# Performance work log

Measured on AMD Instinct MI355X. Metric: run time of the kernel, lower is better.

The kernel has to match this reference:

```python
import jax, jax.numpy as jnp
import numpy as np

EMB = 2048
NQH = 16          # num_q_heads
G = 4             # group_size
NKV = NQH // G    # 4 kv heads
HD = EMB // NQH   # 128 head_dim
B, S = 2, 2048


def setup_inputs() -> dict:
    key = jax.random.key(0)
    ks = jax.random.split(key, 6)
    scale = 1.0 / np.sqrt(EMB)
    x = jax.random.normal(ks[0], (B, S, EMB), dtype=jnp.float32)
    attn_mask = jnp.zeros((B, S), dtype=bool)  # unused placeholder
    # torch Linear weights: (out_features, in_features)
    Wq = jax.random.normal(ks[1], (EMB, EMB), dtype=jnp.float32) * scale
    Wk = jax.random.normal(ks[2], (EMB // G, EMB), dtype=jnp.float32) * scale
    Wv = jax.random.normal(ks[3], (EMB // G, EMB), dtype=jnp.float32) * scale
    Wo = jax.random.normal(ks[4], (EMB, EMB), dtype=jnp.float32) * scale
    return {"x": x, "attn_mask": attn_mask, "is_causal": 1,
            "Wq": Wq, "Wk": Wk, "Wv": Wv, "Wo": Wo}


def reference(x, attn_mask, is_causal, Wq, Wk, Wv, Wo):
    b, n, _ = x.shape
    q = x @ Wq.T                      # (b, n, EMB)
    k = x @ Wk.T                      # (b, n, EMB//G)
    v = x @ Wv.T                      # (b, n, EMB//G)
    # q: b n (h_full d) -> b h_full n d, then (h g) split with h=NKV outer
    q = q.reshape(b, n, NQH, HD).transpose(0, 2, 1, 3)      # (b, NQH, n, d)
    q = q.reshape(b, NKV, G, n, HD).transpose(0, 2, 1, 3, 4)  # (b, g, h, n, d)
    k = k.reshape(b, n, NKV, HD).transpose(0, 2, 1, 3)      # (b, h, s, d)
    v = v.reshape(b, n, NKV, HD).transpose(0, 2, 1, 3)      # (b, h, s, d)
    attn = jnp.einsum('bghnd,bhsd->bghns', q, k) / np.sqrt(HD)
    scores = jax.nn.softmax(attn, axis=-1)  # dropout p=0.0 -> identity
    out = jnp.einsum('bghns,bhsd->bghnd', scores, v)        # (b, g, h, n, d)
    # b g h n d -> b n (h g) d -> b n (h g d)
    out = out.transpose(0, 3, 2, 1, 4).reshape(b, n, EMB)
    y = out @ Wo.T
    return y
```

## Files before the change

### kernel.cpp

```cpp
#include <hip/hip_runtime.h>
#include <stdint.h>


typedef short s8v __attribute__((ext_vector_type(8)));
typedef float f4  __attribute__((ext_vector_type(4)));
typedef unsigned short u16;

#define GLD_LDS(g, l) __builtin_amdgcn_global_load_lds(                     \
    (const __attribute__((address_space(1))) void*)(g),                     \
    (__attribute__((address_space(3))) void*)(l), 16, 0, 0)

__device__ __forceinline__ u16 f2bf(float f) {
    union { float f; uint32_t u; } v; v.f = f;
    uint32_t u = v.u;
    return (u16)((u + 0x7fffu + ((u >> 16) & 1u)) >> 16);
}

__device__ __forceinline__ float fexp2(float x) {
#if __has_builtin(__builtin_amdgcn_exp2f)
    return __builtin_amdgcn_exp2f(x);
#else
    return exp2f(x);
#endif
}

__global__ void cvt_all(const float* __restrict__ x,  const float* __restrict__ wq,
                        const float* __restrict__ wk, const float* __restrict__ wv,
                        const float* __restrict__ wo_,
                        u16* __restrict__ xb, u16* __restrict__ wqkv,
                        u16* __restrict__ wob)
{
    int i = blockIdx.x * blockDim.x + threadIdx.x;
    const float4* s; ushort4* d; int so, dofs;
    if (i < 2097152)      { s = (const float4*)x;   d = (ushort4*)xb;   so = i;           dofs = so; }
    else if (i < 3145728) { s = (const float4*)wq;  d = (ushort4*)wqkv; so = i - 2097152; dofs = so; }
    else if (i < 3407872) { s = (const float4*)wk;  d = (ushort4*)wqkv; so = i - 3145728; dofs = so + 1048576; }
    else if (i < 3670016) { s = (const float4*)wv;  d = (ushort4*)wqkv; so = i - 3407872; dofs = so + 1310720; }
    else                  { s = (const float4*)wo_; d = (ushort4*)wob;  so = i - 3670016; dofs = so; }
    float4 v = s[so];
    ushort4 o;
    o.x = f2bf(v.x); o.y = f2bf(v.y); o.z = f2bf(v.z); o.w = f2bf(v.w);
    d[dofs] = o;
}

template<int MODE>
__global__ __launch_bounds__(512, 1)
void gemm256(const u16* __restrict__ A, const u16* __restrict__ Bm,
             int M, int N, int K,
             u16* __restrict__ qkOut, u16* __restrict__ vtOut,
             float* __restrict__ fOut)
{
    __shared__ __attribute__((aligned(16))) u16 lds[2][2][2][8192];

    const int tid  = threadIdx.x;
    const int lane = tid & 63, quad = lane >> 4, l16 = lane & 15;
    const int wave = tid >> 6;
    const int wr = wave >> 2, wc = wave & 3;

    int bx, by;
    {
        const int nwgx = gridDim.x;
        const int nwg  = nwgx * gridDim.y;
        const int flat = blockIdx.y * nwgx + blockIdx.x;
        const int nflat = (flat & 7) * (nwg >> 3) + (flat >> 3);
        bx = nflat % nwgx; by = nflat / nwgx;
    }
    const int m0 = by * 256, n0 = bx * 256;
    const int NT = K >> 6;

    f4 acc[8][4] = {};

#define VMC6() asm volatile("s_waitcnt vmcnt(6)" ::: "memory")
#define VMC0() asm volatile("s_waitcnt vmcnt(0)" ::: "memory")
#define BAR()  __builtin_amdgcn_s_barrier()

#define STG(bf, op, h, t) if ((t) < NT) {                                   \
        const u16* gb = (op) ? Bm : A;                                      \
        const int rb = ((op) ? n0 : m0) + (h) * 128;                        \
        _Pragma("unroll")                                                   \
        for (int j = 0; j < 2; j++) {                                       \
            int s_ = j * 512 + tid;                                         \
            int r_ = s_ >> 3, cc = s_ & 7;                                  \
            GLD_LDS(gb + (size_t)(rb + r_) * K + (t) * 64                   \
                       + ((cc ^ (r_ & 7)) << 3),                            \
                    &lds[bf][op][h][(j * 512 + (tid & ~63)) * 8]);          \
        } }

#define RD_A(bf, qm, ar) {                                                  \
        _Pragma("unroll")                                                   \
        for (int f = 0; f < 4; f++) {                                       \
            int r_ = (qm) * 64 + f * 16 + l16;                              \
            _Pragma("unroll")                                               \
            for (int kc = 0; kc < 2; kc++)                                  \
                ar[f][kc] = *(const s8v*)(&lds[bf][0][wr]                   \
                    [r_ * 64 + (((kc * 4 + quad) ^ (r_ & 7)) << 3)]);       \
        } }

#define RD_B(bf, qn, br) {                                                  \
        _Pragma("unroll")                                                   \
        for (int f = 0; f < 2; f++) {                                       \
            int r_ = (wc & 1) * 64 + ((qn) * 2 + f) * 16 + l16;             \
            _Pragma("unroll")                                               \
            for (int kc = 0; kc < 2; kc++)                                  \
                br[f][kc] = *(const s8v*)(&lds[bf][1][wc >> 1]              \
                    [r_ * 64 + (((kc * 4 + quad) ^ (r_ & 7)) << 3)]);       \
        } }

#define MM(qm, qn, ar, br) {                                                \
        __builtin_amdgcn_s_setprio(1);                                      \
        _Pragma("unroll")                                                   \
        for (int f = 0; f < 4; f++)                                         \
            _Pragma("unroll")                                               \
            for (int g = 0; g < 2; g++) {                                   \
                acc[(qm)*4+f][(qn)*2+g] = __builtin_amdgcn_mfma_f32_16x16x32_bf16( \
                    ar[f][0], br[g][0], acc[(qm)*4+f][(qn)*2+g], 0, 0, 0);  \
                acc[(qm)*4+f][(qn)*2+g] = __builtin_amdgcn_mfma_f32_16x16x32_bf16( \
                    ar[f][1], br[g][1], acc[(qm)*4+f][(qn)*2+g], 0, 0, 0);  \
            }                                                               \
        __builtin_amdgcn_s_setprio(0); }

    STG(0,1,0,0); STG(0,1,1,0); STG(0,0,0,0); STG(0,0,1,0);
    STG(1,1,0,1); STG(1,1,1,1); STG(1,0,0,1);
    VMC6(); BAR();

    for (int T = 0; T < NT; T += 2) {
        const bool more = (T + 2 < NT);
        s8v a0[4][2], a1[4][2], b0[2][2], b1[2][2];
        RD_A(0,0,a0); RD_B(0,0,b0);
        STG(1,0,1,T+1);
        BAR(); MM(0,0,a0,b0); BAR();
        RD_B(0,1,b1);
        BAR(); MM(0,1,a0,b1); BAR();
        RD_A(0,1,a1);
        STG(0,1,0,T+2);
        BAR(); MM(1,0,a1,b0); BAR();
        STG(0,1,1,T+2); STG(0,0,0,T+2);
        BAR(); MM(1,1,a1,b1);
        if (more) { VMC6(); } else { VMC0(); }
        BAR();
        RD_A(1,0,a0); RD_B(1,0,b0);
        STG(0,0,1,T+2);
        BAR(); MM(0,0,a0,b0); BAR();
        RD_B(1,1,b1);
        BAR(); MM(0,1,a0,b1); BAR();
        RD_A(1,1,a1);
        STG(1,1,0,T+3);
        BAR(); MM(1,0,a1,b0); BAR();
        STG(1,1,1,T+3); STG(1,0,0,T+3);
        BAR(); MM(1,1,a1,b1);
        if (more) { VMC6(); } else { VMC0(); }
        BAR();
    }
#undef STG
#undef RD_A
#undef RD_B
#undef MM

    if (MODE == 0) {
        if (n0 < 2560) {
            const float qs = (n0 < 2048)
                ? (0.08838834764831845f * 1.4426950408889634f) : 1.0f;
            #pragma unroll
            for (int mi = 0; mi < 8; mi++) {
                int gm0 = m0 + wr * 128 + mi * 16 + quad * 4;
                #pragma unroll
                for (int ni = 0; ni < 4; ni++) {
                    int gn = n0 + wc * 64 + ni * 16 + l16;
                    #pragma unroll
                    for (int r = 0; r < 4; r++)
                        qkOut[(size_t)(gm0 + r) * 2560 + gn] = f2bf(acc[mi][ni][r] * qs);
                }
            }
        } else {
            #pragma unroll
            for (int mi = 0; mi < 8; mi++) {
                int gm0 = m0 + wr * 128 + mi * 16 + quad * 4;
                int bb = gm0 >> 11, s = gm0 & 2047;
                #pragma unroll
                for (int ni = 0; ni < 4; ni++) {
                    int gn = n0 + wc * 64 + ni * 16 + l16;
                    int dd = gn - 2560;
                    ushort4 pk;
                    pk.x = f2bf(acc[mi][ni][0]); pk.y = f2bf(acc[mi][ni][1]);
                    pk.z = f2bf(acc[mi][ni][2]); pk.w = f2bf(acc[mi][ni][3]);
                    *(ushort4*)(vtOut +
                        ((size_t)(bb * 4 + (dd >> 7)) * 128 + (dd & 127)) * 2048 + s) = pk;
                }
            }
        }
    } else {
        #pragma unroll
        for (int mi = 0; mi < 8; mi++) {
            int gm0 = m0 + wr * 128 + mi * 16 + quad * 4;
            #pragma unroll
            for (int ni = 0; ni < 4; ni++) {
                int gn = n0 + wc * 64 + ni * 16 + l16;
                #pragma unroll
                for (int r = 0; r < 4; r++)
                    fOut[(size_t)(gm0 + r) * N + gn] = acc[mi][ni][r];
            }
        }
    }
#undef VMC6
#undef VMC0
#undef BAR
}

__global__ __launch_bounds__(512, 1)
void gemm256x128(const u16* __restrict__ A, const u16* __restrict__ Bm,
                 int M, int N, int K, float* __restrict__ fOut)
{
    __shared__ __attribute__((aligned(16))) u16 lds[2][3][8192];

    const int tid  = threadIdx.x;
    const int lane = tid & 63, quad = lane >> 4, l16 = lane & 15;
    const int wave = tid >> 6;
    const int wr = wave >> 2, wc = wave & 3;

    int bx, by;
    {
        const int nwgx = gridDim.x;
        const int nwg  = nwgx * gridDim.y;
        const int flat = blockIdx.y * nwgx + blockIdx.x;
        const int nflat = (flat & 7) * (nwg >> 3) + (flat >> 3);
        bx = nflat % nwgx; by = nflat / nwgx;
    }
    const int m0 = by * 256, n0 = bx * 128;
    const int NT = K >> 6;

    f4 acc[8][2] = {};

#define VMC2() asm volatile("s_waitcnt vmcnt(2)" ::: "memory")
#define VMC0() asm volatile("s_waitcnt vmcnt(0)" ::: "memory")
#define BAR()  __builtin_amdgcn_s_barrier()

#define STG(bf, u, t) if ((t) < NT) {                                       \
        const u16* gb = ((u) == 2) ? Bm : A;                                \
        const int rb = ((u) == 2) ? n0 : (m0 + (u) * 128);                  \
        _Pragma("unroll")                                                   \
        for (int j = 0; j < 2; j++) {                                       \
            int s_ = j * 512 + tid;                                         \
            int r_ = s_ >> 3, cc = s_ & 7;                                  \
            GLD_LDS(gb + (size_t)(rb + r_) * K + (t) * 64                   \
                       + ((cc ^ (r_ & 7)) << 3),                            \
                    &lds[bf][u][(j * 512 + (tid & ~63)) * 8]);              \
        } }

#define RD_A(bf, qm, ar) {                                                  \
        _Pragma("unroll")                                                   \
        for (int f = 0; f < 4; f++) {                                       \
            int r_ = (qm) * 64 + f * 16 + l16;                              \
            _Pragma("unroll")                                               \
            for (int kc = 0; kc < 2; kc++)                                  \
                ar[f][kc] = *(const s8v*)(&lds[bf][wr]                      \
                    [r_ * 64 + (((kc * 4 + quad) ^ (r_ & 7)) << 3)]);       \
        } }

#define RD_B(bf, br) {                                                      \
        _Pragma("unroll")                                                   \
        for (int f = 0; f < 2; f++) {                                       \
            int r_ = wc * 32 + f * 16 + l16;                                \
            _Pragma("unroll")                                               \
            for (int kc = 0; kc < 2; kc++)                                  \
                br[f][kc] = *(const s8v*)(&lds[bf][2]                       \
                    [r_ * 64 + (((kc * 4 + quad) ^ (r_ & 7)) << 3)]);       \
        } }

#define MM(qm, ar, br) {                                                    \
        __builtin_amdgcn_s_setprio(1);                                      \
        _Pragma("unroll")                                                   \
        for (int f = 0; f < 4; f++)                                         \
            _Pragma("unroll")                                               \
            for (int g = 0; g < 2; g++) {                                   \
                acc[(qm)*4+f][g] = __builtin_amdgcn_mfma_f32_16x16x32_bf16( \
                    ar[f][0], br[g][0], acc[(qm)*4+f][g], 0, 0, 0);         \
                acc[(qm)*4+f][g] = __builtin_amdgcn_mfma_f32_16x16x32_bf16( \
                    ar[f][1], br[g][1], acc[(qm)*4+f][g], 0, 0, 0);         \
            }                                                               \
        __builtin_amdgcn_s_setprio(0); }

    STG(0,0,0); STG(0,1,0); STG(0,2,0);
    STG(1,2,1);
    VMC2(); BAR();

    for (int T = 0; T < NT; T += 2) {
        const bool more = (T + 2 < NT);
        s8v a0[4][2], a1[4][2], b[2][2];
        RD_A(0,0,a0); RD_B(0,b);
        STG(1,0,T+1); STG(1,1,T+1);
        BAR(); MM(0,a0,b); BAR();
        RD_A(0,1,a1);
        STG(0,2,T+2);
        BAR(); MM(1,a1,b);
        if (more) { VMC2(); } else { VMC0(); }
        BAR();
        RD_A(1,0,a0); RD_B(1,b);
        STG(0,0,T+2); STG(0,1,T+2);
        BAR(); MM(0,a0,b); BAR();
        RD_A(1,1,a1);
        STG(1,2,T+3);
        BAR(); MM(1,a1,b);
        if (more) { VMC2(); } else { VMC0(); }
        BAR();
    }
#undef STG
#undef RD_A
#undef RD_B
#undef MM
#undef VMC2
#undef VMC0
#undef BAR

    #pragma unroll
    for (int mi = 0; mi < 8; mi++) {
        int gm0 = m0 + wr * 128 + mi * 16 + quad * 4;
        #pragma unroll
        for (int ni = 0; ni < 2; ni++) {
            int gn = n0 + wc * 32 + ni * 16 + l16;
            #pragma unroll
            for (int r = 0; r < 4; r++)
                fOut[(size_t)(gm0 + r) * N + gn] = acc[mi][ni][r];
        }
    }
}

__global__ __launch_bounds__(512, 2)
void attn_kernel(const u16* __restrict__ qk, const u16* __restrict__ vt,
                 u16* __restrict__ ao)
{
    __shared__ __attribute__((aligned(16))) u16 Kb[2][64 * 128];
    __shared__ __attribute__((aligned(16))) u16 Vb[2][128 * 64];
    __shared__ __attribute__((aligned(16))) u16 Ps[8][32 * 72];

    const int tid  = threadIdx.x;
    const int wave = tid >> 6, lane = tid & 63;
    const int quad = lane >> 4, l16 = lane & 15;
    const int bh = blockIdx.x;
    const int b = bh >> 2, h = bh & 3;
    const int hh = wave >> 1, mh = wave & 1;
    const int hq = h * 4 + hh;
    const int qs0 = blockIdx.y * 64;

    s8v aq[2][4];
    #pragma unroll
    for (int mt = 0; mt < 2; mt++) {
        const u16* qrow = qk + (size_t)(b * 2048 + qs0 + (mh * 2 + mt) * 16 + l16) * 2560
                             + hq * 128 + quad * 8;
        #pragma unroll
        for (int c4 = 0; c4 < 4; c4++) aq[mt][c4] = *(const s8v*)(qrow + c4 * 32);
    }

    s8v ones;
    #pragma unroll
    for (int j = 0; j < 8; j++) ones[j] = (short)0x3F80;

    f4 o[2][9] = {};

    const u16* kbase = qk + (size_t)(b * 2048) * 2560 + 2048 + h * 128;
    const u16* vbase = vt + (size_t)bh * 128 * 2048;
    u16* Pw = &Ps[wave][0];

    int bkb[4], bvb[2];
    #pragma unroll
    for (int c4 = 0; c4 < 4; c4++)
        bkb[c4] = l16 * 128 + (((c4 * 4 + quad) ^ (l16 & 7)) * 8);
    #pragma unroll
    for (int kc = 0; kc < 2; kc++)
        bvb[kc] = l16 * 64 + (((kc * 4 + quad) ^ (l16 & 7)) * 8);
    const int apb = l16 * 72 + quad * 8;
    const int psw = l16 * 72 + quad * 4;

#define STAGE(CUR, S) {                                                       \
        _Pragma("unroll")                                                     \
        for (int i = 0; i < 2; i++) {                                         \
            const int c = wave + i * 8;                                       \
            int kr = c * 4 + (lane >> 4);                                     \
            int ksw = (lane & 15) ^ (kr & 7);                                 \
            GLD_LDS(kbase + (size_t)((S) + kr) * 2560 + ksw * 8,              \
                    &Kb[CUR][c * 512]);                                       \
            int vd = c * 8 + (lane >> 3);                                     \
            int vsw = (lane & 7) ^ (vd & 7);                                  \
            GLD_LDS(vbase + (size_t)vd * 2048 + (S) + vsw * 8,                \
                    &Vb[CUR][c * 512]);                                       \
        } }

#define STEP(CUR, S) {                                                        \
        __syncthreads();    \
        if ((S) + 64 < 2048) STAGE((CUR) ^ 1, (S) + 64);                      \
        s8v bk[4][4];                                                         \
        _Pragma("unroll")                                                     \
        for (int c4 = 0; c4 < 4; c4++)                                        \
            _Pragma("unroll")                                                 \
            for (int cg = 0; cg < 4; cg++)                                    \
                bk[c4][cg] = *(const s8v*)(&Kb[CUR][bkb[c4] + cg * 2048]);    \
        _Pragma("unroll")                                                     \
        for (int mt = 0; mt < 2; mt++) {                                      \
            f4 sc[4] = {};                                                    \
            _Pragma("unroll")                                                 \
            for (int c4 = 0; c4 < 4; c4++)                                    \
                _Pragma("unroll")                                             \
                for (int cg = 0; cg < 4; cg++)                                \
                    sc[cg] = __builtin_amdgcn_mfma_f32_16x16x32_bf16(         \
                        bk[c4][cg], aq[mt][c4], sc[cg], 0, 0, 0);             \
               \
            _Pragma("unroll")                                                 \
            for (int cg = 0; cg < 4; cg++) {                                  \
                ushort4 pk;                                                   \
                pk.x = (u16)(__float_as_uint(fexp2(sc[cg][0])) >> 16);        \
                pk.y = (u16)(__float_as_uint(fexp2(sc[cg][1])) >> 16);        \
                pk.z = (u16)(__float_as_uint(fexp2(sc[cg][2])) >> 16);        \
                pk.w = (u16)(__float_as_uint(fexp2(sc[cg][3])) >> 16);        \
                *(ushort4*)(Pw + psw + mt * 1152 + cg * 16) = pk;             \
            }                                                                 \
        }                                                                     \
        s8v ap[2][2];                                                         \
        _Pragma("unroll")                                                     \
        for (int mt = 0; mt < 2; mt++)                                        \
            _Pragma("unroll")                                                 \
            for (int kc = 0; kc < 2; kc++)                                    \
                ap[mt][kc] = *(const s8v*)(Pw + apb + mt * 1152 + kc * 32);   \
        _Pragma("unroll")                                                     \
        for (int ch = 0; ch < 8; ch++) {                                      \
            s8v bv0 = *(const s8v*)(&Vb[CUR][bvb[0] + ch * 1024]);            \
            s8v bv1 = *(const s8v*)(&Vb[CUR][bvb[1] + ch * 1024]);            \
            _Pragma("unroll")                                                 \
            for (int mt = 0; mt < 2; mt++) {                                  \
                o[mt][ch] = __builtin_amdgcn_mfma_f32_16x16x32_bf16(          \
                    ap[mt][0], bv0, o[mt][ch], 0, 0, 0);                      \
                o[mt][ch] = __builtin_amdgcn_mfma_f32_16x16x32_bf16(          \
                    ap[mt][1], bv1, o[mt][ch], 0, 0, 0);                      \
            }                                                                 \
        }                                                                     \
        _Pragma("unroll")                                                     \
        for (int mt = 0; mt < 2; mt++) {                                      \
            o[mt][8] = __builtin_amdgcn_mfma_f32_16x16x32_bf16(               \
                ap[mt][0], ones, o[mt][8], 0, 0, 0);                          \
            o[mt][8] = __builtin_amdgcn_mfma_f32_16x16x32_bf16(               \
                ap[mt][1], ones, o[mt][8], 0, 0, 0);                          \
        } }

    STAGE(0, 0);
    for (int s0 = 0; s0 < 2048; s0 += 128) {
        STEP(0, s0);
        STEP(1, s0 + 64);
    }
#undef STEP
#undef STAGE

    #pragma unroll
    for (int mt = 0; mt < 2; mt++)
        #pragma unroll
        for (int r = 0; r < 4; r++) {
            float inv = 1.f / o[mt][8][r];
            int gm = b * 2048 + qs0 + (mh * 2 + mt) * 16 + quad * 4 + r;
            #pragma unroll
            for (int ch = 0; ch < 8; ch++)
                ao[(size_t)gm * 2048 + hq * 128 + ch * 16 + l16] =
                    f2bf(o[mt][ch][r] * inv);
        }
}

extern "C" void kernel_launch(void* const* d_in, const int* in_sizes, int n_in,
                              void* d_out, int out_size, void* d_ws, size_t ws_size,
                              hipStream_t stream)
{
    const float* x  = (const float*)d_in[0];
    const float* Wq = (const float*)d_in[3];
    const float* Wk = (const float*)d_in[4];
    const float* Wv = (const float*)d_in[5];
    const float* Wo = (const float*)d_in[6];

    char* ws = (char*)d_ws;
    u16* xb   = (u16*)(ws);
    u16* wqkv = (u16*)(ws + 16777216);
    u16* wo   = (u16*)(ws + 29360128);
    u16* qkb  = (u16*)(ws + 37748736);
    u16* vtb  = (u16*)(ws + 58720256);
    u16* ao   = (u16*)(ws + 62914560);
    if (ws_size < 79691776u) return;

    cvt_all<<<18432, 256, 0, stream>>>(x, Wq, Wk, Wv, Wo, xb, wqkv, wo);

    gemm256<0><<<dim3(12, 16), 512, 0, stream>>>(xb, wqkv, 4096, 3072, 2048,
                                                 qkb, vtb, nullptr);
    attn_kernel<<<dim3(8, 32), 512, 0, stream>>>(qkb, vtb, ao);
    gemm256x128<<<dim3(16, 16), 512, 0, stream>>>(ao, wo, 4096, 2048, 2048,
                                                  (float*)d_out);
}
```

Measured before the change: 278.9 us.

## Retile QKV projection GEMM to 256x192 tiles for 256 workgroups

Replaces the 256x256-tile QKV GEMM (192 workgroups) with a 256x192-tile variant launched as 16x16 = 256 workgroups, matching the CU count better to reduce tail imbalance. The B-operand staging, LDS layout, wait counts and MFMA schedule are restructured for three 16-wide column fragments per wave, and the epilogue now selects Q scaling, K store, or transposed V store per 16-column fragment. Smaller N tile lowers arithmetic intensity per workgroup and changes the barrier/load pipeline schedule.

Result: faster. 268.0 us (-3.9%).

```diff
diff --git a/kernel.cpp b/kernel.cpp
--- a/kernel.cpp
+++ b/kernel.cpp
@@ -43,14 +43,13 @@
     d[dofs] = o;
 }
 
-template<int MODE>
 __global__ __launch_bounds__(512, 1)
-void gemm256(const u16* __restrict__ A, const u16* __restrict__ Bm,
-             int M, int N, int K,
-             u16* __restrict__ qkOut, u16* __restrict__ vtOut,
-             float* __restrict__ fOut)
+void gemm256x192(const u16* __restrict__ A, const u16* __restrict__ Bm,
+                 int K,
+                 u16* __restrict__ qkOut, u16* __restrict__ vtOut)
 {
-    __shared__ __attribute__((aligned(16))) u16 lds[2][2][2][8192];
+    __shared__ __attribute__((aligned(16))) u16 ldsA[2][2][8192];
+    __shared__ __attribute__((aligned(16))) u16 ldsB[2][12288];
 
     const int tid  = threadIdx.x;
     const int lane = tid & 63, quad = lane >> 4, l16 = lane & 15;
@@ -65,25 +64,33 @@
         const int nflat = (flat & 7) * (nwg >> 3) + (flat >> 3);
         bx = nflat % nwgx; by = nflat / nwgx;
     }
-    const int m0 = by * 256, n0 = bx * 256;
+    const int m0 = by * 256, n0 = bx * 192;
     const int NT = K >> 6;
 
-    f4 acc[8][4] = {};
-
-#define VMC6() asm volatile("s_waitcnt vmcnt(6)" ::: "memory")
+    f4 acc[8][3] = {};
+
+#define VMC3() asm volatile("s_waitcnt vmcnt(3)" ::: "memory")
 #define VMC0() asm volatile("s_waitcnt vmcnt(0)" ::: "memory")
 #define BAR()  __builtin_amdgcn_s_barrier()
 
-#define STG(bf, op, h, t) if ((t) < NT) {                                   \
-        const u16* gb = (op) ? Bm : A;                                      \
-        const int rb = ((op) ? n0 : m0) + (h) * 128;                        \
+#define STGA(bf, h, t) if ((t) < NT) {                                      \
         _Pragma("unroll")                                                   \
         for (int j = 0; j < 2; j++) {                                       \
             int s_ = j * 512 + tid;                                         \
             int r_ = s_ >> 3, cc = s_ & 7;                                  \
-            GLD_LDS(gb + (size_t)(rb + r_) * K + (t) * 64                   \
+            GLD_LDS(A + (size_t)(m0 + (h) * 128 + r_) * K + (t) * 64        \
+                      + ((cc ^ (r_ & 7)) << 3),                             \
+                    &ldsA[bf][h][(j * 512 + (tid & ~63)) * 8]);             \
+        } }
+
+#define STGB(bf, t) if ((t) < NT) {                                         \
+        _Pragma("unroll")                                                   \
+        for (int j = 0; j < 3; j++) {                                       \
+            int s_ = j * 512 + tid;                                         \
+            int r_ = s_ >> 3, cc = s_ & 7;                                  \
+            GLD_LDS(Bm + (size_t)(n0 + r_) * K + (t) * 64                   \
                        + ((cc ^ (r_ & 7)) << 3),                            \
-                    &lds[bf][op][h][(j * 512 + (tid & ~63)) * 8]);          \
+                    &ldsB[bf][(j * 512 + (tid & ~63)) * 8]);                \
         } }
 
 #define RD_A(bf, qm, ar) {                                                  \
@@ -92,118 +99,93 @@
             int r_ = (qm) * 64 + f * 16 + l16;                              \
             _Pragma("unroll")                                               \
             for (int kc = 0; kc < 2; kc++)                                  \
-                ar[f][kc] = *(const s8v*)(&lds[bf][0][wr]                   \
+                ar[f][kc] = *(const s8v*)(&ldsA[bf][wr]                     \
                     [r_ * 64 + (((kc * 4 + quad) ^ (r_ & 7)) << 3)]);       \
         } }
 
-#define RD_B(bf, qn, br) {                                                  \
-        _Pragma("unroll")                                                   \
-        for (int f = 0; f < 2; f++) {                                       \
-            int r_ = (wc & 1) * 64 + ((qn) * 2 + f) * 16 + l16;             \
+#define RD_B(bf, br) {                                                      \
+        _Pragma("unroll")                                                   \
+        for (int f = 0; f < 3; f++) {                                       \
+            int r_ = wc * 48 + f * 16 + l16;                                \
             _Pragma("unroll")                                               \
             for (int kc = 0; kc < 2; kc++)                                  \
-                br[f][kc] = *(const s8v*)(&lds[bf][1][wc >> 1]              \
+                br[f][kc] = *(const s8v*)(&ldsB[bf]                         \
                     [r_ * 64 + (((kc * 4 + quad) ^ (r_ & 7)) << 3)]);       \
         } }
 
-#define MM(qm, qn, ar, br) {                                                \
+#define MM(qm, ar, br) {                                                    \
         __builtin_amdgcn_s_setprio(1);                                      \
         _Pragma("unroll")                                                   \
         for (int f = 0; f < 4; f++)                                         \
             _Pragma("unroll")                                               \
-            for (int g = 0; g < 2; g++) {                                   \
-                acc[(qm)*4+f][(qn)*2+g] = __builtin_amdgcn_mfma_f32_16x16x32_bf16( \
-                    ar[f][0], br[g][0], acc[(qm)*4+f][(qn)*2+g], 0, 0, 0);  \
-                acc[(qm)*4+f][(qn)*2+g] = __builtin_amdgcn_mfma_f32_16x16x32_bf16( \
-                    ar[f][1], br[g][1], acc[(qm)*4+f][(qn)*2+g], 0, 0, 0);  \
+            for (int g = 0; g < 3; g++) {                                   \
+                acc[(qm)*4+f][g] = __builtin_amdgcn_mfma_f32_16x16x32_bf16( \
+                    ar[f][0], br[g][0], acc[(qm)*4+f][g], 0, 0, 0);         \
+                acc[(qm)*4+f][g] = __builtin_amdgcn_mfma_f32_16x16x32_bf16( \
+                    ar[f][1], br[g][1], acc[(qm)*4+f][g], 0, 0, 0);         \
             }                                                               \
         __builtin_amdgcn_s_setprio(0); }
 
-    STG(0,1,0,0); STG(0,1,1,0); STG(0,0,0,0); STG(0,0,1,0);
-    STG(1,1,0,1); STG(1,1,1,1); STG(1,0,0,1);
-    VMC6(); BAR();
+    STGA(0,0,0); STGA(0,1,0); STGB(0,0);
+    STGB(1,1);
+    VMC3(); BAR();
 
     for (int T = 0; T < NT; T += 2) {
         const bool more = (T + 2 < NT);
-        s8v a0[4][2], a1[4][2], b0[2][2], b1[2][2];
-        RD_A(0,0,a0); RD_B(0,0,b0);
-        STG(1,0,1,T+1);
-        BAR(); MM(0,0,a0,b0); BAR();
-        RD_B(0,1,b1);
-        BAR(); MM(0,1,a0,b1); BAR();
+        s8v a0[4][2], a1[4][2], b[3][2];
+        RD_A(0,0,a0); RD_B(0,b);
+        STGA(1,0,T+1); STGA(1,1,T+1);
+        BAR(); MM(0,a0,b); BAR();
         RD_A(0,1,a1);
-        STG(0,1,0,T+2);
-        BAR(); MM(1,0,a1,b0); BAR();
-        STG(0,1,1,T+2); STG(0,0,0,T+2);
-        BAR(); MM(1,1,a1,b1);
-        if (more) { VMC6(); } else { VMC0(); }
+        STGB(0,T+2);
+        BAR(); MM(1,a1,b);
+        if (more) { VMC3(); } else { VMC0(); }
         BAR();
-        RD_A(1,0,a0); RD_B(1,0,b0);
-        STG(0,0,1,T+2);
-        BAR(); MM(0,0,a0,b0); BAR();
-        RD_B(1,1,b1);
-        BAR(); MM(0,1,a0,b1); BAR();
+        RD_A(1,0,a0); RD_B(1,b);
+        STGA(0,0,T+2); STGA(0,1,T+2);
+        BAR(); MM(0,a0,b); BAR();
         RD_A(1,1,a1);
-        STG(1,1,0,T+3);
-        BAR(); MM(1,0,a1,b0); BAR();
-        STG(1,1,1,T+3); STG(1,0,0,T+3);
-        BAR(); MM(1,1,a1,b1);
-        if (more) { VMC6(); } else { VMC0(); }
+        STGB(1,T+3);
+        BAR(); MM(1,a1,b);
+        if (more) { VMC3(); } else { VMC0(); }
         BAR();
     }
-#undef STG
+#undef STGA
+#undef STGB
 #undef RD_A
 #undef RD_B
 #undef MM
-
-    if (MODE == 0) {
-        if (n0 < 2560) {
-            const float qs = (n0 < 2048)
-                ? (0.08838834764831845f * 1.4426950408889634f) : 1.0f;
-            #pragma unroll
-            for (int mi = 0; mi < 8; mi++) {
-                int gm0 = m0 + wr * 128 + mi * 16 + quad * 4;
+#undef VMC3
+#undef VMC0
+#undef BAR
+
+    const float qs = 0.08838834764831845f * 1.4426950408889634f;
+    #pragma unroll
+    for (int mi = 0; mi < 8; mi++) {
+        int gm0 = m0 + wr * 128 + mi * 16 + quad * 4;
+        int bb = gm0 >> 11, s = gm0 & 2047;
+        #pragma unroll
+        for (int ni = 0; ni < 3; ni++) {
+            int base = n0 + wc * 48 + ni * 16;
+            int gn = base + l16;
+            if (base < 2048) {
                 #pragma unroll
-                for (int ni = 0; ni < 4; ni++) {
-                    int gn = n0 + wc * 64 + ni * 16 + l16;
-                    #pragma unroll
-                    for (int r = 0; r < 4; r++)
-                        qkOut[(size_t)(gm0 + r) * 2560 + gn] = f2bf(acc[mi][ni][r] * qs);
-                }
-            }
-        } else {
-            #pragma unroll
-            for (int mi = 0; mi < 8; mi++) {
-                int gm0 = m0 + wr * 128 + mi * 16 + quad * 4;
-                int bb = gm0 >> 11, s = gm0 & 2047;
+                for (int r = 0; r < 4; r++)
+                    qkOut[(size_t)(gm0 + r) * 2560 + gn] = f2bf(acc[mi][ni][r] * qs);
+            } else if (base < 2560) {
                 #pragma unroll
-                for (int ni = 0; ni < 4; ni++) {
-                    int gn = n0 + wc * 64 + ni * 16 + l16;
-                    int dd = gn - 2560;
-                    ushort4 pk;
-                    pk.x = f2bf(acc[mi][ni][0]); pk.y = f2bf(acc[mi][ni][1]);
-                    pk.z = f2bf(acc[mi][ni][2]); pk.w = f2bf(acc[mi][ni][3]);
-                    *(ushort4*)(vtOut +
-                        ((size_t)(bb * 4 + (dd >> 7)) * 128 + (dd & 127)) * 2048 + s) = pk;
-                }
+                for (int r = 0; r < 4; r++)
+                    qkOut[(size_t)(gm0 + r) * 2560 + gn] = f2bf(acc[mi][ni][r]);
+            } else {
+                int dd = gn - 2560;
+                ushort4 pk;
+                pk.x = f2bf(acc[mi][ni][0]); pk.y = f2bf(acc[mi][ni][1]);
+                pk.z = f2bf(acc[mi][ni][2]); pk.w = f2bf(acc[mi][ni][3]);
+                *(ushort4*)(vtOut +
+                    ((size_t)(bb * 4 + (dd >> 7)) * 128 + (dd & 127)) * 2048 + s) = pk;
             }
         }
-    } else {
-        #pragma unroll
-        for (int mi = 0; mi < 8; mi++) {
-            int gm0 = m0 + wr * 128 + mi * 16 + quad * 4;
-            #pragma unroll
-            for (int ni = 0; ni < 4; ni++) {
-                int gn = n0 + wc * 64 + ni * 16 + l16;
-                #pragma unroll
-                for (int r = 0; r < 4; r++)
-                    fOut[(size_t)(gm0 + r) * N + gn] = acc[mi][ni][r];
-            }
-        }
-    }
-#undef VMC6
-#undef VMC0
-#undef BAR
+    }
 }
 
 __global__ __launch_bounds__(512, 1)
@@ -402,7 +384,6 @@
                 for (int cg = 0; cg < 4; cg++)                                \
                     sc[cg] = __builtin_amdgcn_mfma_f32_16x16x32_bf16(         \
                         bk[c4][cg], aq[mt][c4], sc[cg], 0, 0, 0);             \
-               \
             _Pragma("unroll")                                                 \
             for (int cg = 0; cg < 4; cg++) {                                  \
                 ushort4 pk;                                                   \
@@ -481,8 +462,7 @@
 
     cvt_all<<<18432, 256, 0, stream>>>(x, Wq, Wk, Wv, Wo, xb, wqkv, wo);
 
-    gemm256<0><<<dim3(12, 16), 512, 0, stream>>>(xb, wqkv, 4096, 3072, 2048,
-                                                 qkb, vtb, nullptr);
+    gemm256x192<<<dim3(16, 16), 512, 0, stream>>>(xb, wqkv, 2048, qkb, vtb);
     attn_kernel<<<dim3(8, 32), 512, 0, stream>>>(qkb, vtb, ao);
     gemm256x128<<<dim3(16, 16), 512, 0, stream>>>(ao, wo, 4096, 2048, 2048,
                                                   (float*)d_out);
```
